# Kernel tuning notes

Hardware: AMD Instinct MI355X
Metric: run time of the kernel (lower is better)

## Reference

```python
import jax, jax.numpy as jnp
import numpy as np

N_EMBD, N_HEAD, HEAD_DIM = 1024, 16, 64
N_EXPERTS, TOP_K, EXPERT_DIM = 8, 2, 2048
EPS = 1e-5


def rmsnorm(x):
    return x * jax.lax.rsqrt(jnp.mean(x * x, axis=-1, keepdims=True) + EPS)


def setup_inputs() -> dict:
    key = jax.random.key(0)
    ks = jax.random.split(key, 9)
    s = 0.02
    x = jax.random.normal(ks[0], (2, 2048, N_EMBD), dtype=jnp.float32)
    # weights stored [in, out] (torch Linear applies x @ W.T; we pre-transpose)
    wq = jax.random.normal(ks[1], (N_EMBD, N_EMBD), dtype=jnp.float32) * s
    wk = jax.random.normal(ks[2], (N_EMBD, N_EMBD), dtype=jnp.float32) * s
    wv = jax.random.normal(ks[3], (N_EMBD, N_EMBD), dtype=jnp.float32) * s
    wo = jax.random.normal(ks[4], (N_EMBD, N_EMBD), dtype=jnp.float32) * s
    router_w = jax.random.normal(ks[5], (N_EMBD, N_EXPERTS), dtype=jnp.float32) * s
    exp_fc1 = jax.random.normal(ks[6], (N_EXPERTS, N_EMBD, EXPERT_DIM), dtype=jnp.float32) * s
    exp_fc2 = jax.random.normal(ks[7], (N_EXPERTS, EXPERT_DIM, N_EMBD), dtype=jnp.float32) * s
    return {"x": x, "wq": wq, "wk": wk, "wv": wv, "wo": wo,
            "router_w": router_w, "exp_fc1": exp_fc1, "exp_fc2": exp_fc2}


def _attn(h, wq, wk, wv, wo):
    B, T, C = h.shape
    sc = 1.0 / np.sqrt(HEAD_DIM)
    q = (h @ wq).reshape(B, T, N_HEAD, HEAD_DIM)
    k = (h @ wk).reshape(B, T, N_HEAD, HEAD_DIM)
    v = (h @ wv).reshape(B, T, N_HEAD, HEAD_DIM)
    s = jnp.einsum('bqhd,bkhd->bhqk', q, k) * sc
    causal = jnp.triu(jnp.ones((T, T), dtype=bool), 1)
    s = jnp.where(causal, -jnp.inf, s)
    a = jax.nn.softmax(s, axis=-1)
    o = jnp.einsum('bhqk,bkhd->bqhd', a, v).reshape(B, T, C)
    return o @ wo


def _moe(h, router_w, exp_fc1, exp_fc2):
    B, T, D = h.shape
    xf = h.reshape(B * T, D)
    probs = jax.nn.softmax(xf @ router_w, axis=-1)          # [N, E]
    top_vals, top_idx = jax.lax.top_k(probs, TOP_K)          # [N, K]
    top_vals = top_vals / jnp.sum(top_vals, axis=-1, keepdims=True)
    # combine weight per (token, expert); top_k indices are distinct
    combine = jnp.sum(jax.nn.one_hot(top_idx, N_EXPERTS, dtype=xf.dtype)
                      * top_vals[..., None], axis=1)         # [N, E]
    h1 = jnp.square(jax.nn.relu(jnp.einsum('nd,edh->neh', xf, exp_fc1)))
    oe = jnp.einsum('neh,ehd->ned', h1, exp_fc2)             # [N, E, D]
    out = jnp.einsum('ned,ne->nd', oe, combine)
    return out.reshape(B, T, D)


def reference(x, wq, wk, wv, wo, router_w, exp_fc1, exp_fc2):
    x = x + _attn(rmsnorm(x), wq, wk, wv, wo)
    x = x + _moe(rmsnorm(x), router_w, exp_fc1, exp_fc2)
    return x
```

## Files before the change

kernel.cpp:

```cpp
#include <hip/hip_runtime.h>
#include <math.h>

#define NTOK 4096
#define DEMB 1024
#define TSEQ 2048
#define QKVS 3072
#define QKN  2048
#define EDIM 2048
#define NEXP 8

typedef unsigned short u16;
typedef unsigned int u32;
typedef __bf16 bf16_t;
typedef __bf16 bf16x8 __attribute__((ext_vector_type(8)));
typedef __bf16 bf16x4 __attribute__((ext_vector_type(4)));
typedef float f32x4 __attribute__((ext_vector_type(4)));

__device__ __forceinline__ f32x4 mfma16(bf16x8 a, bf16x8 b, f32x4 c) {
    return __builtin_amdgcn_mfma_f32_16x16x32_bf16(a, b, c, 0, 0, 0);
}
__device__ __forceinline__ void gll16(const void* g, void* l) {
    __builtin_amdgcn_global_load_lds((const __attribute__((address_space(1))) u32*)g,
                                     (__attribute__((address_space(3))) u32*)l, 16, 0, 0);
}
__device__ __forceinline__ u16 f2bf(float x) {
    union { __bf16 h; u16 u; } c; c.h = (__bf16)x; return c.u;
}

__global__ __launch_bounds__(256) void rmsnorm_split_k(const float* __restrict__ x,
                                                       bf16_t* __restrict__ hi,
                                                       bf16_t* __restrict__ lo) {
    const int row = blockIdx.x;
    const float4 v = ((const float4*)(x + (size_t)row * DEMB))[threadIdx.x];
    float ss = v.x*v.x + v.y*v.y + v.z*v.z + v.w*v.w;
    #pragma unroll
    for (int off = 32; off; off >>= 1) ss += __shfl_xor(ss, off);
    __shared__ float wsum[4];
    if ((threadIdx.x & 63) == 0) wsum[threadIdx.x >> 6] = ss;
    __syncthreads();
    const float r = rsqrtf((wsum[0]+wsum[1]+wsum[2]+wsum[3]) * (1.0f/DEMB) + 1e-5f);
    const float f[4] = {v.x*r, v.y*r, v.z*r, v.w*r};
    bf16x4 hv, lv;
    #pragma unroll
    for (int j = 0; j < 4; j++) {
        const __bf16 hb = (__bf16)f[j];
        hv[j] = hb;
        lv[j] = (__bf16)(f[j] - (float)hb);
    }
    ((bf16x4*)(hi + (size_t)row*DEMB))[threadIdx.x] = hv;
    ((bf16x4*)(lo + (size_t)row*DEMB))[threadIdx.x] = lv;
}

__global__ __launch_bounds__(256) void transp_split_k(const float* __restrict__ w,
                                                      bf16_t* __restrict__ wth,
                                                      bf16_t* __restrict__ wtl,
                                                      int K, int M) {
    __shared__ float t[32][33];
    const int m0 = blockIdx.x*32, k0 = blockIdx.y*32;
    const int tx = threadIdx.x & 31, ty = threadIdx.x >> 5;
    #pragma unroll
    for (int i = 0; i < 32; i += 8) t[ty+i][tx] = w[(size_t)(k0+ty+i)*M + m0+tx];
    __syncthreads();
    #pragma unroll
    for (int i = 0; i < 32; i += 8) {
        const float f = t[tx][ty+i];
        const __bf16 hb = (__bf16)f;
        wth[(size_t)(m0+ty+i)*K + k0+tx] = hb;
        wtl[(size_t)(m0+ty+i)*K + k0+tx] = (__bf16)(f - (float)hb);
    }
}

__global__ __launch_bounds__(256) void transp_k(const float* __restrict__ w,
                                                bf16_t* __restrict__ wt,
                                                int K, int M) {
    __shared__ float t[32][33];
    const size_t eo = (size_t)blockIdx.z * K * M;
    w += eo; wt += eo;
    const int m0 = blockIdx.x*32, k0 = blockIdx.y*32;
    const int tx = threadIdx.x & 31, ty = threadIdx.x >> 5;
    #pragma unroll
    for (int i = 0; i < 32; i += 8) t[ty+i][tx] = w[(size_t)(k0+ty+i)*M + m0+tx];
    __syncthreads();
    #pragma unroll
    for (int i = 0; i < 32; i += 8) wt[(size_t)(m0+ty+i)*K + k0+tx] = (__bf16)t[tx][ty+i];
}

__global__ __launch_bounds__(512) void gemm_qkv256(const bf16_t* __restrict__ Ah,
                                                   const bf16_t* __restrict__ Al,
                                                   const bf16_t* __restrict__ Bh,
                                                   const bf16_t* __restrict__ Bl,
                                                   bf16_t* __restrict__ qkh,
                                                   bf16_t* __restrict__ qkl,
                                                   bf16_t* __restrict__ vth,
                                                   bf16_t* __restrict__ vtl) {
    __shared__ u16 As[2*16384];
    __shared__ u16 Bs[2*16384];
    const int tid = threadIdx.x;
    const int lane = tid & 63, w = tid >> 6;
    const int lr = lane & 15, lg = lane >> 4;
    const int wm = w >> 2, wn = w & 3;
    int flat = blockIdx.y * 12 + blockIdx.x;
    flat = (flat & 7) * 24 + (flat >> 3);
    const int m0 = (flat / 12) * 256, n0 = (flat % 12) * 256;

    const int srow = tid >> 3;
    const int sd   = (tid & 7) ^ (srow & 7);
    const int kofs = (sd & 3) * 8;
    const bf16_t* Asrc = (sd < 4) ? Ah : Al;
    const bf16_t* Bsrc = (sd < 4) ? Bh : Bl;
    const bf16_t* pA0 = Asrc + (size_t)(m0 + srow      ) * 1024 + kofs;
    const bf16_t* pA1 = Asrc + (size_t)(m0 + srow +  64) * 1024 + kofs;
    const bf16_t* pA2 = Asrc + (size_t)(m0 + srow + 128) * 1024 + kofs;
    const bf16_t* pA3 = Asrc + (size_t)(m0 + srow + 192) * 1024 + kofs;
    const bf16_t* pB0 = Bsrc + (size_t)(n0 + srow      ) * 1024 + kofs;
    const bf16_t* pB1 = Bsrc + (size_t)(n0 + srow +  64) * 1024 + kofs;
    const bf16_t* pB2 = Bsrc + (size_t)(n0 + srow + 128) * 1024 + kofs;
    const bf16_t* pB3 = Bsrc + (size_t)(n0 + srow + 192) * 1024 + kofs;
    const int ca = (lg ^ (lr & 7)) * 8;

#define STG_Q(u_, kn_, nb_) do { \
    gll16(pA##u_ + (kn_), (char*)As + (nb_)*32768 + (u_)*8192 + tid*16); \
    gll16(pB##u_ + (kn_), (char*)Bs + (nb_)*32768 + (u_)*8192 + tid*16); } while (0)

    STG_Q(0, 0, 0); STG_Q(1, 0, 0); STG_Q(2, 0, 0); STG_Q(3, 0, 0);
    asm volatile("s_waitcnt vmcnt(0)" ::: "memory");
    __builtin_amdgcn_sched_barrier(0);
    __syncthreads();

    f32x4 acc[8][4] = {};
    int cur = 0;
    for (int t = 0; t < 32; t++) {
        const u16* Ab = As + cur*16384;
        const u16* Bb = Bs + cur*16384;
        const int nb = cur ^ 1;
        const int kn = (t + 1) * 32;
        const bool more = (t < 31);

        bf16x8 bh[4], bl[4];
        #pragma unroll
        for (int j = 0; j < 4; j++) {
            const int bo = (wn*64 + j*16 + lr)*64 + ca;
            bh[j] = *(const bf16x8*)&Bb[bo];
            bl[j] = *(const bf16x8*)&Bb[bo ^ 32];
        }
        {
            bf16x8 ah[4], al[4];
            #pragma unroll
            for (int i = 0; i < 4; i++) {
                const int ao = (wm*128 + i*16 + lr)*64 + ca;
                ah[i] = *(const bf16x8*)&Ab[ao];
                al[i] = *(const bf16x8*)&Ab[ao ^ 32];
            }
            if (more) { STG_Q(0, kn, nb); STG_Q(1, kn, nb); }
            __builtin_amdgcn_s_barrier();
            asm volatile("s_waitcnt lgkmcnt(0)" ::: "memory");
            __builtin_amdgcn_sched_barrier(0);
            __builtin_amdgcn_s_setprio(1);
            #pragma unroll
            for (int i = 0; i < 4; i++)
                #pragma unroll
                for (int j = 0; j < 4; j++) {
                    acc[i][j] = mfma16(ah[i], bh[j], acc[i][j]);
                    acc[i][j] = mfma16(ah[i], bl[j], acc[i][j]);
                    acc[i][j] = mfma16(al[i], bh[j], acc[i][j]);
                }
            __builtin_amdgcn_s_setprio(0);
            __builtin_amdgcn_s_barrier();
        }
        {
            bf16x8 ah[4], al[4];
            #pragma unroll
            for (int i = 0; i < 4; i++) {
                const int ao = (wm*128 + 64 + i*16 + lr)*64 + ca;
                ah[i] = *(const bf16x8*)&Ab[ao];
                al[i] = *(const bf16x8*)&Ab[ao ^ 32];
            }
            if (more) { STG_Q(2, kn, nb); STG_Q(3, kn, nb); }
            __builtin_amdgcn_s_barrier();
            asm volatile("s_waitcnt lgkmcnt(0)" ::: "memory");
            __builtin_amdgcn_sched_barrier(0);
            __builtin_amdgcn_s_setprio(1);
            #pragma unroll
            for (int i = 0; i < 4; i++)
                #pragma unroll
                for (int j = 0; j < 4; j++) {
                    acc[4+i][j] = mfma16(ah[i], bh[j], acc[4+i][j]);
                    acc[4+i][j] = mfma16(ah[i], bl[j], acc[4+i][j]);
                    acc[4+i][j] = mfma16(al[i], bh[j], acc[4+i][j]);
                }
            __builtin_amdgcn_s_setprio(0);
            asm volatile("s_waitcnt vmcnt(0)" ::: "memory");
            __builtin_amdgcn_sched_barrier(0);
            __builtin_amdgcn_s_barrier();
        }
        cur ^= 1;
    }
#undef STG_Q
    #pragma unroll
    for (int i = 0; i < 8; i++) {
        #pragma unroll
        for (int j = 0; j < 4; j++) {
            const int row = m0 + wm*128 + i*16 + lg*4;
            const int col = n0 + wn*64 + j*16 + lr;
            const f32x4 v = acc[i][j];
            if (col < QKN) {
                const float sc = (col < DEMB) ? 0.125f : 1.0f;
                #pragma unroll
                for (int r = 0; r < 4; r++) {
                    const size_t o = (size_t)(row + r) * QKN + col;
                    const float f = v[r] * sc;
                    const __bf16 hb = (__bf16)f;
                    qkh[o] = hb;
                    qkl[o] = (__bf16)(f - (float)hb);
                }
            } else {
                const int d = col - QKN;
                const int hh = d >> 6, dd = d & 63;
                const int bb = row >> 11, tt = row & 2047;
                const size_t base = ((size_t)(bb*16 + hh)*64 + dd) * TSEQ + tt;
                #pragma unroll
                for (int r = 0; r < 4; r++) {
                    const float f = v[r];
                    const __bf16 hb = (__bf16)f;
                    vth[base + r] = hb;
                    vtl[base + r] = (__bf16)(f - (float)hb);
                }
            }
        }
    }
}

template<int EPI>
__global__ __launch_bounds__(256) void gemm_split(const bf16_t* __restrict__ Ah,
                                                  const bf16_t* __restrict__ Al,
                                                  const bf16_t* __restrict__ Bh,
                                                  const bf16_t* __restrict__ Bl,
                                                  const float* __restrict__ res,
                                                  float* __restrict__ C,
                                                  int N, int K) {
    __shared__ u16 As[16384];
    __shared__ u16 Bs[16384];
    const int tid = threadIdx.x;
    const int lane = tid & 63, w = tid >> 6;
    const int lr = lane & 15, lg = lane >> 4;
    const int wm = w >> 1, wn = w & 1;
    const int nbx = gridDim.x;
    const int nwg = gridDim.x * gridDim.y;
    int flat = blockIdx.y * nbx + blockIdx.x;
    flat = (flat & 7) * (nwg >> 3) + (flat >> 3);
    const int m0 = (flat / nbx) * 128, n0 = (flat % nbx) * 128;

    const int srow = tid >> 3;
    const int sd   = (tid & 7) ^ (srow & 7);
    const int kofs = (sd & 3) * 8;
    const bf16_t* Asrc = (sd < 4) ? Ah : Al;
    const bf16_t* Bsrc = (sd < 4) ? Bh : Bl;
    const bf16_t* pa0 = Asrc + (size_t)(m0 + srow     ) * K + kofs;
    const bf16_t* pa1 = Asrc + (size_t)(m0 + srow + 32) * K + kofs;
    const bf16_t* pa2 = Asrc + (size_t)(m0 + srow + 64) * K + kofs;
    const bf16_t* pa3 = Asrc + (size_t)(m0 + srow + 96) * K + kofs;
    const bf16_t* pb0 = Bsrc + (size_t)(n0 + srow     ) * K + kofs;
    const bf16_t* pb1 = Bsrc + (size_t)(n0 + srow + 32) * K + kofs;
    const bf16_t* pb2 = Bsrc + (size_t)(n0 + srow + 64) * K + kofs;
    const bf16_t* pb3 = Bsrc + (size_t)(n0 + srow + 96) * K + kofs;
    char* dA = (char*)As + tid*16;
    char* dB = (char*)Bs + tid*16;
    const int ca = (lg ^ (lr & 7)) * 8;

    auto STG = [&](int bsel, int kk) {
        char* a_ = dA + bsel*16384;
        char* b_ = dB + bsel*16384;
        gll16(pa0 + kk, a_);          gll16(pa1 + kk, a_ + 4096);
        gll16(pa2 + kk, a_ + 8192);   gll16(pa3 + kk, a_ + 12288);
        gll16(pb0 + kk, b_);          gll16(pb1 + kk, b_ + 4096);
        gll16(pb2 + kk, b_ + 8192);   gll16(pb3 + kk, b_ + 12288);
    };

    STG(0, 0);
    asm volatile("s_waitcnt vmcnt(0)" ::: "memory");
    __syncthreads();
    f32x4 acc[4][4] = {};
    int cur = 0;
    for (int k0 = 0; k0 < K; k0 += 32) {
        if (k0 + 32 < K) STG(cur ^ 1, k0 + 32);
        const u16* Ab = As + cur*8192;
        const u16* Bb = Bs + cur*8192;
        bf16x8 ah[4], al[4], bh[4], bl[4];
        #pragma unroll
        for (int i = 0; i < 4; i++) {
            const int ao = (wm*64 + i*16 + lr)*64 + ca;
            const int bo = (wn*64 + i*16 + lr)*64 + ca;
            ah[i] = *(const bf16x8*)&Ab[ao];
            al[i] = *(const bf16x8*)&Ab[ao ^ 32];
            bh[i] = *(const bf16x8*)&Bb[bo];
            bl[i] = *(const bf16x8*)&Bb[bo ^ 32];
        }
        #pragma unroll
        for (int i = 0; i < 4; i++)
            #pragma unroll
            for (int j = 0; j < 4; j++) {
                acc[i][j] = mfma16(ah[i], bh[j], acc[i][j]);
                acc[i][j] = mfma16(ah[i], bl[j], acc[i][j]);
                acc[i][j] = mfma16(al[i], bh[j], acc[i][j]);
            }
        asm volatile("s_waitcnt vmcnt(0)" ::: "memory");
        __syncthreads();
        cur ^= 1;
    }
    #pragma unroll
    for (int i = 0; i < 4; i++) {
        #pragma unroll
        for (int j = 0; j < 4; j++) {
            const int row = m0 + wm*64 + i*16 + lg*4;
            const int col = n0 + wn*64 + j*16 + lr;
            const f32x4 v = acc[i][j];
            #pragma unroll
            for (int r = 0; r < 4; r++) {
                const size_t o = (size_t)(row + r) * N + col;
                C[o] = res[o] + v[r];
            }
        }
    }
}

template<int EPI, int GATHER>
__global__ __launch_bounds__(256) void gemm_moe(const bf16_t* __restrict__ A,
                                                const bf16_t* __restrict__ Ball,
                                                bf16_t* __restrict__ C,
                                                const int* __restrict__ rowmap,
                                                const int* __restrict__ counts,
                                                const int* __restrict__ offs,
                                                int N, int K) {
    const int e = blockIdx.z;
    const int cnt = counts[e];
    if ((int)blockIdx.y * 128 >= cnt) return;
    const int base = offs[e];
    const bf16_t* Bt = Ball + (size_t)e * N * K;
    __shared__ u16 As[8192];
    __shared__ u16 Bs[8192];
    const int tid = threadIdx.x;
    const int lane = tid & 63, w = tid >> 6;
    const int lr = lane & 15, lg = lane >> 4;
    const int wm = w >> 1, wn = w & 1;
    const int m0 = blockIdx.y * 128, n0 = blockIdx.x * 128;

    const int srp = tid >> 3;
    const int sd  = (tid & 7) ^ (srp & 7);
    const int smrow = 2*srp + (sd >> 2);
    const int kofs  = (sd & 3) * 8;
    const int l0 = min(m0 + smrow, cnt - 1), l1 = min(m0 + 64 + smrow, cnt - 1);
    const size_t r0 = GATHER ? (size_t)rowmap[base + l0] : (size_t)(base + l0);
    const size_t r1 = GATHER ? (size_t)rowmap[base + l1] : (size_t)(base + l1);
    const bf16_t* pa0 = A + r0 * K + kofs;
    const bf16_t* pa1 = A + r1 * K + kofs;
    const bf16_t* pb0 = Bt + (size_t)(n0 + smrow)      * K + kofs;
    const bf16_t* pb1 = Bt + (size_t)(n0 + 64 + smrow) * K + kofs;
    char* dA = (char*)As + tid*16;
    char* dB = (char*)Bs + tid*16;
    const int cs = (((lr & 1) << 2) + lg) ^ ((lr >> 1) & 7);

    auto STG = [&](int bsel, int kk) {
        char* a_ = dA + bsel*8192;
        char* b_ = dB + bsel*8192;
        gll16(pa0 + kk, a_); gll16(pa1 + kk, a_ + 4096);
        gll16(pb0 + kk, b_); gll16(pb1 + kk, b_ + 4096);
    };

    STG(0, 0);
    asm volatile("s_waitcnt vmcnt(0)" ::: "memory");
    __syncthreads();
    f32x4 acc[4][4] = {};
    int cur = 0;
    for (int k0 = 0; k0 < K; k0 += 32) {
        if (k0 + 32 < K) STG(cur ^ 1, k0 + 32);
        const u16* Ab = As + cur*4096;
        const u16* Bb = Bs + cur*4096;
        bf16x8 af[4], bfr[4];
        #pragma unroll
        for (int i = 0; i < 4; i++) {
            af[i]  = *(const bf16x8*)&Ab[(wm*32 + i*8 + (lr>>1))*64 + cs*8];
            bfr[i] = *(const bf16x8*)&Bb[(wn*32 + i*8 + (lr>>1))*64 + cs*8];
        }
        #pragma unroll
        for (int i = 0; i < 4; i++)
            #pragma unroll
            for (int j = 0; j < 4; j++)
                acc[i][j] = mfma16(af[i], bfr[j], acc[i][j]);
        asm volatile("s_waitcnt vmcnt(0)" ::: "memory");
        __syncthreads();
        cur ^= 1;
    }
    #pragma unroll
    for (int i = 0; i < 4; i++) {
        #pragma unroll
        for (int j = 0; j < 4; j++) {
            const int rowl = m0 + wm*64 + i*16 + lg*4;
            const int col  = n0 + wn*64 + j*16 + lr;
            const f32x4 v = acc[i][j];
            #pragma unroll
            for (int r = 0; r < 4; r++) {
                if (rowl + r < cnt) {
                    float xv = v[r];
                    if (EPI == 2) { xv = fmaxf(xv, 0.f); xv = xv * xv; }
                    C[(size_t)(base + rowl + r) * N + col] = (__bf16)xv;
                }
            }
        }
    }
}

__global__ __launch_bounds__(256) void attn_mfma(const bf16_t* __restrict__ qkh,
                                                 const bf16_t* __restrict__ qkl,
                                                 const bf16_t* __restrict__ vth,
                                                 const bf16_t* __restrict__ vtl,
                                                 bf16_t* __restrict__ aoh,
                                                 bf16_t* __restrict__ aol) {
    __shared__ u16 KsH[64*64];
    __shared__ u16 KsL[64*64];
    __shared__ u16 VtH[64*64];
    __shared__ u16 VtL[64*64];
    __shared__ u16 P_H[4*16*72];
    __shared__ u16 P_L[4*16*72];
    const int tid = threadIdx.x, lane = tid & 63, wv = tid >> 6;
    const int lr = lane & 15, lg = lane >> 4;
    const int L = blockIdx.x + blockIdx.y*16 + blockIdx.z*256;
    const int swz = (L & 7)*64 + (L >> 3);
    const int qa = swz & 15;
    const int h  = (swz >> 4) & 15;
    const int b  = swz >> 8;
    const int qb = 31 - qa;
    u16* plwH = P_H + wv * 16 * 72;
    u16* plwL = P_L + wv * 16 * 72;
    const int wq0A = qa*64 + wv*16;
    const int wq0B = qb*64 + wv*16;

    bf16x8 qAh[2], qAl[2], qBh[2], qBl[2];
    #pragma unroll
    for (int kf = 0; kf < 2; kf++) {
        const size_t qoA = (size_t)(b*TSEQ + wq0A + lr)*QKN + h*64 + kf*32 + lg*8;
        const size_t qoB = (size_t)(b*TSEQ + wq0B + lr)*QKN + h*64 + kf*32 + lg*8;
        qAh[kf] = *(const bf16x8*)(qkh + qoA);
        qAl[kf] = *(const bf16x8*)(qkl + qoA);
        qBh[kf] = *(const bf16x8*)(qkh + qoB);
        qBl[kf] = *(const bf16x8*)(qkl + qoB);
    }

    f32x4 ofA[4] = {}, ofB[4] = {};
    float mA = -1e30f, lA = 0.f, mB = -1e30f, lB = 0.f;

    const int skv = tid >> 3;
    const int pst = tid & 7;
    const int chs = pst ^ (skv & 7);
    const int bh = b*16 + h;
    const bf16_t* kh = qkh + 1024;
    const bf16_t* kl = qkl + 1024;
    const size_t vrow0 = (size_t)(bh*64 + skv)      * TSEQ;
    const size_t vrow1 = (size_t)(bh*64 + skv + 32) * TSEQ;

    auto step = [&](f32x4 (&of)[4], float& mrun, float& lrun,
                    const bf16x8 (&qfh)[2], const bf16x8 (&qfl)[2],
                    const int wq0, const bool diag, const int kvb) {
        f32x4 sf[4] = {};
        #pragma unroll
        for (int kf = 0; kf < 2; kf++)
            #pragma unroll
            for (int f = 0; f < 4; f++) {
                const int idx = (f*16 + lr)*64 + ((kf*32 + lg*8) ^ ((lr & 7) << 3));
                const bf16x8 ah = *(const bf16x8*)&KsH[idx];
                const bf16x8 al = *(const bf16x8*)&KsL[idx];
                sf[f] = mfma16(ah, qfh[kf], sf[f]);
                sf[f] = mfma16(ah, qfl[kf], sf[f]);
                sf[f] = mfma16(al, qfh[kf], sf[f]);
            }
        if (diag) {
            #pragma unroll
            for (int f = 0; f < 4; f++)
                #pragma unroll
                for (int r = 0; r < 4; r++)
                    if (kvb + f*16 + lg*4 + r > wq0 + lr) sf[f][r] = -1e30f;
        }
        float tm = -1e30f;
        #pragma unroll
        for (int f = 0; f < 4; f++)
            tm = fmaxf(tm, fmaxf(fmaxf(sf[f][0], sf[f][1]), fmaxf(sf[f][2], sf[f][3])));
        tm = fmaxf(tm, __shfl_xor(tm, 16));
        tm = fmaxf(tm, __shfl_xor(tm, 32));
        const float mnew = fmaxf(mrun, tm);
        const float fac = __expf(mrun - mnew);
        mrun = mnew;
        float ps = 0.f;
        #pragma unroll
        for (int f = 0; f < 4; f++) {
            float p[4];
            #pragma unroll
            for (int r = 0; r < 4; r++) { p[r] = __expf(sf[f][r] - mnew); ps += p[r]; }
            u16 hb4[4], lb4[4];
            #pragma unroll
            for (int r = 0; r < 4; r++) {
                const __bf16 hbv = (__bf16)p[r];
                hb4[r] = f2bf(p[r]);
                lb4[r] = f2bf(p[r] - (float)hbv);
            }
            u32* pwh = (u32*)&plwH[lr*72 + f*16 + lg*4];
            u32* pwl = (u32*)&plwL[lr*72 + f*16 + lg*4];
            pwh[0] = (u32)hb4[0] | ((u32)hb4[1] << 16);
            pwh[1] = (u32)hb4[2] | ((u32)hb4[3] << 16);
            pwl[0] = (u32)lb4[0] | ((u32)lb4[1] << 16);
            pwl[1] = (u32)lb4[2] | ((u32)lb4[3] << 16);
        }
        ps += __shfl_xor(ps, 16);
        ps += __shfl_xor(ps, 32);
        lrun = lrun*fac + ps;
        #pragma unroll
        for (int f2 = 0; f2 < 4; f2++)
            #pragma unroll
            for (int r = 0; r < 4; r++) of[f2][r] *= fac;
        #pragma unroll
        for (int hf = 0; hf < 2; hf++) {
            const bf16x8 pbh = *(const bf16x8*)&plwH[lr*72 + hf*32 + lg*8];
            const bf16x8 pbl = *(const bf16x8*)&plwL[lr*72 + hf*32 + lg*8];
            #pragma unroll
            for (int f2 = 0; f2 < 4; f2++) {
                const int vidx = (f2*16 + lr)*64 + (((hf*4 + lg) ^ (lr & 7)) << 3);
                const bf16x8 vah = *(const bf16x8*)&VtH[vidx];
                const bf16x8 val = *(const bf16x8*)&VtL[vidx];
                of[f2] = mfma16(vah, pbh, of[f2]);
                of[f2] = mfma16(vah, pbl, of[f2]);
                of[f2] = mfma16(val, pbh, of[f2]);
            }
        }
    };

    for (int kt = 0; kt <= qb; kt++) {
        __syncthreads();
        const size_t krow = (size_t)(b*TSEQ + kt*64 + skv)*QKN + h*64;
        gll16(kh + krow + chs*8,                     (char*)KsH + tid*16);
        gll16(kh + krow + (size_t)32*QKN + chs*8,    (char*)KsH + 4096 + tid*16);
        gll16(kl + krow + chs*8,                     (char*)KsL + tid*16);
        gll16(kl + krow + (size_t)32*QKN + chs*8,    (char*)KsL + 4096 + tid*16);
        gll16(vth + vrow0 + kt*64 + chs*8,           (char*)VtH + tid*16);
        gll16(vth + vrow1 + kt*64 + chs*8,           (char*)VtH + 4096 + tid*16);
        gll16(vtl + vrow0 + kt*64 + chs*8,           (char*)VtL + tid*16);
        gll16(vtl + vrow1 + kt*64 + chs*8,           (char*)VtL + 4096 + tid*16);
        __syncthreads();
        if (kt <= qa) step(ofA, mA, lA, qAh, qAl, wq0A, kt == qa, kt*64);
        step(ofB, mB, lB, qBh, qBl, wq0B, kt == qb, kt*64);
    }

    const float invA = 1.f / lA, invB = 1.f / lB;
    #pragma unroll
    for (int f2 = 0; f2 < 4; f2++) {
        u16 hb4[4], lb4[4];
        #pragma unroll
        for (int r = 0; r < 4; r++) {
            const float f = ofA[f2][r] * invA;
            const __bf16 hbv = (__bf16)f;
            hb4[r] = f2bf(f);
            lb4[r] = f2bf(f - (float)hbv);
        }
        u32* pwh = (u32*)&plwH[lr*72 + f2*16 + lg*4];
        u32* pwl = (u32*)&plwL[lr*72 + f2*16 + lg*4];
        pwh[0] = (u32)hb4[0] | ((u32)hb4[1] << 16);
        pwh[1] = (u32)hb4[2] | ((u32)hb4[3] << 16);
        pwl[0] = (u32)lb4[0] | ((u32)lb4[1] << 16);
        pwl[1] = (u32)lb4[2] | ((u32)lb4[3] << 16);
    }
    asm volatile("s_waitcnt lgkmcnt(0)" ::: "memory");
    __builtin_amdgcn_sched_barrier(0);
    #pragma unroll
    for (int pass = 0; pass < 2; pass++) {
        const int qlr = pass*8 + (lane >> 3);
        const int ch = (lane & 7) * 8;
        const bf16x8 oh = *(const bf16x8*)&plwH[qlr*72 + ch];
        const bf16x8 ol = *(const bf16x8*)&plwL[qlr*72 + ch];
        const size_t go = (size_t)(b*TSEQ + wq0A + qlr) * DEMB + h*64 + ch;
        *(bf16x8*)(aoh + go) = oh;
        *(bf16x8*)(aol + go) = ol;
    }
    asm volatile("s_waitcnt lgkmcnt(0)" ::: "memory");
    __builtin_amdgcn_sched_barrier(0);
    #pragma unroll
    for (int f2 = 0; f2 < 4; f2++) {
        u16 hb4[4], lb4[4];
        #pragma unroll
        for (int r = 0; r < 4; r++) {
            const float f = ofB[f2][r] * invB;
            const __bf16 hbv = (__bf16)f;
            hb4[r] = f2bf(f);
            lb4[r] = f2bf(f - (float)hbv);
        }
        u32* pwh = (u32*)&plwH[lr*72 + f2*16 + lg*4];
        u32* pwl = (u32*)&plwL[lr*72 + f2*16 + lg*4];
        pwh[0] = (u32)hb4[0] | ((u32)hb4[1] << 16);
        pwh[1] = (u32)hb4[2] | ((u32)hb4[3] << 16);
        pwl[0] = (u32)lb4[0] | ((u32)lb4[1] << 16);
        pwl[1] = (u32)lb4[2] | ((u32)lb4[3] << 16);
    }
    asm volatile("s_waitcnt lgkmcnt(0)" ::: "memory");
    __builtin_amdgcn_sched_barrier(0);
    #pragma unroll
    for (int pass = 0; pass < 2; pass++) {
        const int qlr = pass*8 + (lane >> 3);
        const int ch = (lane & 7) * 8;
        const bf16x8 oh = *(const bf16x8*)&plwH[qlr*72 + ch];
        const bf16x8 ol = *(const bf16x8*)&plwL[qlr*72 + ch];
        const size_t go = (size_t)(b*TSEQ + wq0B + qlr) * DEMB + h*64 + ch;
        *(bf16x8*)(aoh + go) = oh;
        *(bf16x8*)(aol + go) = ol;
    }
}

__global__ void zero8(int* c) { if (threadIdx.x < NEXP) c[threadIdx.x] = 0; }

__global__ __launch_bounds__(256) void router_k(const float* __restrict__ xout,
                                                const float* __restrict__ rw,
                                                bf16_t* __restrict__ h,
                                                int* __restrict__ idx,
                                                float* __restrict__ wts,
                                                int* __restrict__ pos,
                                                int* __restrict__ counts) {
    const int tok = blockIdx.x * 4 + (threadIdx.x >> 6);
    const int lane = threadIdx.x & 63;
    const float* xr = xout + (size_t)tok * DEMB;
    float xv16[16];
    float ss = 0.f;
    float acc[NEXP];
    #pragma unroll
    for (int e = 0; e < NEXP; e++) acc[e] = 0.f;
    #pragma unroll
    for (int i = 0; i < 16; i++) {
        const int kk = lane + i*64;
        const float xv = xr[kk];
        xv16[i] = xv;
        ss += xv * xv;
        #pragma unroll
        for (int e = 0; e < NEXP; e++) acc[e] += xv * rw[kk*NEXP + e];
    }
    #pragma unroll
    for (int off = 32; off; off >>= 1) ss += __shfl_xor(ss, off);
    #pragma unroll
    for (int e = 0; e < NEXP; e++) {
        #pragma unroll
        for (int off = 32; off; off >>= 1) acc[e] += __shfl_xor(acc[e], off);
    }
    const float r = rsqrtf(ss * (1.0f/DEMB) + 1e-5f);
    #pragma unroll
    for (int i = 0; i < 16; i++)
        h[(size_t)tok*DEMB + lane + i*64] = (__bf16)(xv16[i] * r);
    if (lane == 0) {
        float v[NEXP];
        #pragma unroll
        for (int e = 0; e < NEXP; e++) v[e] = acc[e] * r;
        int b0 = 0; float v0 = v[0];
        #pragma unroll
        for (int e = 1; e < NEXP; e++) if (v[e] > v0) { v0 = v[e]; b0 = e; }
        int b1 = -1; float v1 = -1e30f;
        #pragma unroll
        for (int e = 0; e < NEXP; e++) if (e != b0 && v[e] > v1) { v1 = v[e]; b1 = e; }
        const float w0 = 1.f / (1.f + __expf(v1 - v0));
        idx[tok*2+0] = b0; idx[tok*2+1] = b1;
        wts[tok*2+0] = w0; wts[tok*2+1] = 1.f - w0;
        pos[tok*2+0] = atomicAdd(&counts[b0], 1);
        pos[tok*2+1] = atomicAdd(&counts[b1], 1);
    }
}

__global__ void offsets_k(const int* __restrict__ counts, int* __restrict__ offs) {
    if (threadIdx.x == 0) {
        int s = 0;
        for (int e = 0; e < NEXP; e++) { offs[e] = s; s += counts[e]; }
    }
}

__global__ __launch_bounds__(256) void buildmap_k(const int* __restrict__ idx,
                                                  const int* __restrict__ pos,
                                                  const int* __restrict__ offs,
                                                  int* __restrict__ rowmap,
                                                  int* __restrict__ rowpos) {
    const int n = blockIdx.x * 256 + threadIdx.x;
    #pragma unroll
    for (int s = 0; s < 2; s++) {
        const int e = idx[n*2+s];
        const int r = offs[e] + pos[n*2+s];
        rowmap[r] = n;
        rowpos[n*2+s] = r;
    }
}

__global__ __launch_bounds__(256) void combine_k(const bf16_t* __restrict__ oe,
                                                 const int* __restrict__ rowpos,
                                                 const float* __restrict__ wts,
                                                 float* __restrict__ out) {
    const int n = blockIdx.x;
    const int r0 = rowpos[n*2+0], r1 = rowpos[n*2+1];
    const float w0 = wts[n*2+0], w1 = wts[n*2+1];
    const int c = threadIdx.x * 4;
    const bf16x4 a  = *(const bf16x4*)(oe + (size_t)r0*DEMB + c);
    const bf16x4 b4 = *(const bf16x4*)(oe + (size_t)r1*DEMB + c);
    float4* op = (float4*)(out + (size_t)n*DEMB + c);
    float4 o = *op;
    o.x += w0*(float)a[0] + w1*(float)b4[0];
    o.y += w0*(float)a[1] + w1*(float)b4[1];
    o.z += w0*(float)a[2] + w1*(float)b4[2];
    o.w += w0*(float)a[3] + w1*(float)b4[3];
    *op = o;
}

extern "C" void kernel_launch(void* const* d_in, const int* in_sizes, int n_in,
                              void* d_out, int out_size, void* d_ws, size_t ws_size,
                              hipStream_t stream) {
    (void)in_sizes; (void)n_in; (void)out_size; (void)ws_size;
    const float* x   = (const float*)d_in[0];
    const float* wq  = (const float*)d_in[1];
    const float* wk  = (const float*)d_in[2];
    const float* wv  = (const float*)d_in[3];
    const float* wo  = (const float*)d_in[4];
    const float* rw  = (const float*)d_in[5];
    const float* fc1 = (const float*)d_in[6];
    const float* fc2 = (const float*)d_in[7];
    float* out = (float*)d_out;
    char* ws = (char*)d_ws;
    const size_t MB = 1024*1024;

    bf16_t* wqkv_h = (bf16_t*)(ws);
    bf16_t* wqkv_l = (bf16_t*)(ws + 6*MB);
    bf16_t* wo_h   = (bf16_t*)(ws + 12*MB);
    bf16_t* wo_l   = (bf16_t*)(ws + 14*MB);
    bf16_t* qk_h   = (bf16_t*)(ws + 16*MB);
    bf16_t* qk_l   = (bf16_t*)(ws + 32*MB);
    bf16_t* vt_h   = (bf16_t*)(ws + 48*MB);
    bf16_t* vt_l   = (bf16_t*)(ws + 56*MB);
    bf16_t* fc1_t  = (bf16_t*)(ws + 16*MB);
    bf16_t* fc2_t  = (bf16_t*)(ws + 48*MB);
    bf16_t* h_hi   = (bf16_t*)(ws + 64*MB);
    bf16_t* h_lo   = (bf16_t*)(ws + 72*MB);
    bf16_t* ao_h   = (bf16_t*)(ws + 64*MB);
    bf16_t* ao_l   = (bf16_t*)(ws + 72*MB);
    bf16_t* h      = (bf16_t*)(ws + 80*MB);
    bf16_t* h1     = (bf16_t*)(ws + 88*MB);
    bf16_t* oe     = (bf16_t*)(ws);
    char* meta = ws + 120*MB;
    int*   idx    = (int*)(meta);
    int*   pos    = (int*)(meta + 64*1024);
    int*   rowmap = (int*)(meta + 128*1024);
    int*   rowpos = (int*)(meta + 192*1024);
    float* wts    = (float*)(meta + 256*1024);
    int*   counts = (int*)(meta + 320*1024);
    int*   offs   = (int*)(meta + 320*1024 + 256);

    const dim3 blk(256);

    transp_split_k<<<dim3(32,32), blk, 0, stream>>>(wq, wqkv_h,               wqkv_l,               1024, 1024);
    transp_split_k<<<dim3(32,32), blk, 0, stream>>>(wk, wqkv_h + 1024*1024,   wqkv_l + 1024*1024,   1024, 1024);
    transp_split_k<<<dim3(32,32), blk, 0, stream>>>(wv, wqkv_h + 2*1024*1024, wqkv_l + 2*1024*1024, 1024, 1024);
    transp_split_k<<<dim3(32,32), blk, 0, stream>>>(wo, wo_h,                 wo_l,                 1024, 1024);
    rmsnorm_split_k<<<NTOK, blk, 0, stream>>>(x, h_hi, h_lo);
    gemm_qkv256<<<dim3(12, 16), dim3(512), 0, stream>>>(
        h_hi, h_lo, wqkv_h, wqkv_l, qk_h, qk_l, vt_h, vt_l);
    attn_mfma<<<dim3(16, 16, 2), blk, 0, stream>>>(qk_h, qk_l, vt_h, vt_l, ao_h, ao_l);
    gemm_split<1><<<dim3(DEMB/128, NTOK/128), blk, 0, stream>>>(
        ao_h, ao_l, wo_h, wo_l, x, out, DEMB, 1024);

    transp_k<<<dim3(64,32,8), blk, 0, stream>>>(fc1, fc1_t, 1024, 2048);
    transp_k<<<dim3(32,64,8), blk, 0, stream>>>(fc2, fc2_t, 2048, 1024);
    zero8<<<1, 64, 0, stream>>>(counts);
    router_k<<<NTOK/4, blk, 0, stream>>>(out, rw, h, idx, wts, pos, counts);
    offsets_k<<<1, 64, 0, stream>>>(counts, offs);
    buildmap_k<<<NTOK/256, blk, 0, stream>>>(idx, pos, offs, rowmap, rowpos);
    gemm_moe<2,1><<<dim3(EDIM/128, 32, NEXP), blk, 0, stream>>>(
        h, fc1_t, h1, rowmap, counts, offs, EDIM, 1024);
    gemm_moe<3,0><<<dim3(DEMB/128, 32, NEXP), blk, 0, stream>>>(
        h1, fc2_t, oe, rowmap, counts, offs, DEMB, EDIM);
    combine_k<<<NTOK, blk, 0, stream>>>(oe, rowpos, wts, out);
}
```

Before: 507.9 us.

## Replace atomic routing and map kernels with single-block deterministic scan scheduler

Removes the zero, offsets and buildmap kernels and the per-token atomics. A single 256-thread block now does a shared-memory prefix scan over expert assignments to build counts, offsets, rowmap and rowpos. This cuts three launches and the atomic contention, and it also makes row order deterministic. The router also switches to contiguous per-lane loads and vectorized bf16x8 stores. The trade-off is a serial single-block kernel with a log-step scan on the critical path.

```diff
diff --git a/kernel.cpp b/kernel.cpp
--- a/kernel.cpp
+++ b/kernel.cpp
@@ -610,31 +610,25 @@
     }
 }
 
-__global__ void zero8(int* c) { if (threadIdx.x < NEXP) c[threadIdx.x] = 0; }
-
 __global__ __launch_bounds__(256) void router_k(const float* __restrict__ xout,
                                                 const float* __restrict__ rw,
                                                 bf16_t* __restrict__ h,
                                                 int* __restrict__ idx,
-                                                float* __restrict__ wts,
-                                                int* __restrict__ pos,
-                                                int* __restrict__ counts) {
+                                                float* __restrict__ wts) {
     const int tok = blockIdx.x * 4 + (threadIdx.x >> 6);
     const int lane = threadIdx.x & 63;
-    const float* xr = xout + (size_t)tok * DEMB;
-    float xv16[16];
+    const float* xr = xout + (size_t)tok * DEMB + lane*16;
+    float xv[16];
     float ss = 0.f;
     float acc[NEXP];
     #pragma unroll
     for (int e = 0; e < NEXP; e++) acc[e] = 0.f;
     #pragma unroll
     for (int i = 0; i < 16; i++) {
-        const int kk = lane + i*64;
-        const float xv = xr[kk];
-        xv16[i] = xv;
-        ss += xv * xv;
-        #pragma unroll
-        for (int e = 0; e < NEXP; e++) acc[e] += xv * rw[kk*NEXP + e];
+        xv[i] = xr[i];
+        ss += xv[i]*xv[i];
+        #pragma unroll
+        for (int e = 0; e < NEXP; e++) acc[e] += xv[i] * rw[(lane*16 + i)*NEXP + e];
     }
     #pragma unroll
     for (int off = 32; off; off >>= 1) ss += __shfl_xor(ss, off);
@@ -644,9 +638,14 @@
         for (int off = 32; off; off >>= 1) acc[e] += __shfl_xor(acc[e], off);
     }
     const float r = rsqrtf(ss * (1.0f/DEMB) + 1e-5f);
-    #pragma unroll
-    for (int i = 0; i < 16; i++)
-        h[(size_t)tok*DEMB + lane + i*64] = (__bf16)(xv16[i] * r);
+    bf16x8 o0, o1;
+    #pragma unroll
+    for (int j = 0; j < 8; j++) {
+        o0[j] = (__bf16)(xv[j] * r);
+        o1[j] = (__bf16)(xv[8+j] * r);
+    }
+    *(bf16x8*)(h + (size_t)tok*DEMB + lane*16)     = o0;
+    *(bf16x8*)(h + (size_t)tok*DEMB + lane*16 + 8) = o1;
     if (lane == 0) {
         float v[NEXP];
         #pragma unroll
@@ -660,30 +659,64 @@
         const float w0 = 1.f / (1.f + __expf(v1 - v0));
         idx[tok*2+0] = b0; idx[tok*2+1] = b1;
         wts[tok*2+0] = w0; wts[tok*2+1] = 1.f - w0;
-        pos[tok*2+0] = atomicAdd(&counts[b0], 1);
-        pos[tok*2+1] = atomicAdd(&counts[b1], 1);
-    }
-}
-
-__global__ void offsets_k(const int* __restrict__ counts, int* __restrict__ offs) {
-    if (threadIdx.x == 0) {
+    }
+}
+
+__global__ __launch_bounds__(256) void sched_k(const int* __restrict__ idx,
+                                               int* __restrict__ counts,
+                                               int* __restrict__ offs,
+                                               int* __restrict__ rowmap,
+                                               int* __restrict__ rowpos) {
+    __shared__ int bufA[NEXP][256];
+    __shared__ int bufB[NEXP][256];
+    __shared__ int runb[256][NEXP];
+    __shared__ int offv[NEXP];
+    const int t = threadIdx.x;
+    int myidx[32];
+    #pragma unroll
+    for (int i = 0; i < 32; i++) myidx[i] = idx[t*32 + i];
+    #pragma unroll
+    for (int e = 0; e < NEXP; e++) runb[t][e] = 0;
+    #pragma unroll
+    for (int i = 0; i < 32; i++) runb[t][myidx[i]]++;
+    #pragma unroll
+    for (int e = 0; e < NEXP; e++) bufA[e][t] = runb[t][e];
+    __syncthreads();
+    int (*cur)[256] = bufA;
+    int (*nxt)[256] = bufB;
+    for (int d = 1; d < 256; d <<= 1) {
+        #pragma unroll
+        for (int e = 0; e < NEXP; e++) {
+            int v = cur[e][t];
+            if (t >= d) v += cur[e][t - d];
+            nxt[e][t] = v;
+        }
+        __syncthreads();
+        int (*tmp)[256] = cur; cur = nxt; nxt = tmp;
+    }
+    if (t == 0) {
         int s = 0;
-        for (int e = 0; e < NEXP; e++) { offs[e] = s; s += counts[e]; }
-    }
-}
-
-__global__ __launch_bounds__(256) void buildmap_k(const int* __restrict__ idx,
-                                                  const int* __restrict__ pos,
-                                                  const int* __restrict__ offs,
-                                                  int* __restrict__ rowmap,
-                                                  int* __restrict__ rowpos) {
-    const int n = blockIdx.x * 256 + threadIdx.x;
-    #pragma unroll
-    for (int s = 0; s < 2; s++) {
-        const int e = idx[n*2+s];
-        const int r = offs[e] + pos[n*2+s];
-        rowmap[r] = n;
-        rowpos[n*2+s] = r;
+        #pragma unroll
+        for (int e = 0; e < NEXP; e++) {
+            const int c = cur[e][255];
+            counts[e] = c;
+            offs[e] = s;
+            offv[e] = s;
+            s += c;
+        }
+    }
+    __syncthreads();
+    #pragma unroll
+    for (int e = 0; e < NEXP; e++) {
+        const int excl = (t == 0) ? 0 : cur[e][t-1];
+        runb[t][e] = offv[e] + excl;
+    }
+    #pragma unroll
+    for (int i = 0; i < 32; i++) {
+        const int e = myidx[i];
+        const int r = runb[t][e]++;
+        rowmap[r] = (t*32 + i) >> 1;
+        rowpos[t*32 + i] = r;
     }
 }
 
@@ -741,7 +774,6 @@
     bf16_t* oe     = (bf16_t*)(ws);
     char* meta = ws + 120*MB;
     int*   idx    = (int*)(meta);
-    int*   pos    = (int*)(meta + 64*1024);
     int*   rowmap = (int*)(meta + 128*1024);
     int*   rowpos = (int*)(meta + 192*1024);
     float* wts    = (float*)(meta + 256*1024);
@@ -763,10 +795,8 @@
 
     transp_k<<<dim3(64,32,8), blk, 0, stream>>>(fc1, fc1_t, 1024, 2048);
     transp_k<<<dim3(32,64,8), blk, 0, stream>>>(fc2, fc2_t, 2048, 1024);
-    zero8<<<1, 64, 0, stream>>>(counts);
-    router_k<<<NTOK/4, blk, 0, stream>>>(out, rw, h, idx, wts, pos, counts);
-    offsets_k<<<1, 64, 0, stream>>>(counts, offs);
-    buildmap_k<<<NTOK/256, blk, 0, stream>>>(idx, pos, offs, rowmap, rowpos);
+    router_k<<<NTOK/4, blk, 0, stream>>>(out, rw, h, idx, wts);
+    sched_k<<<1, blk, 0, stream>>>(idx, counts, offs, rowmap, rowpos);
     gemm_moe<2,1><<<dim3(EDIM/128, 32, NEXP), blk, 0, stream>>>(
         h, fc1_t, h1, rowmap, counts, offs, EDIM, 1024);
     gemm_moe<3,0><<<dim3(DEMB/128, 32, NEXP), blk, 0, stream>>>(
```

Measured after the change: 430.1 us. 1.18x faster.
